# Optimization experiments

Measured on AMD Instinct MI355X. Metric: run time of the kernel, lower is better.

Reference implementation:

```python
import jax, jax.numpy as jnp
import numpy as np

C = 512
C8 = C // 8  # 64
B, H, W = 4, 64, 64


def setup_inputs() -> dict:
    key = jax.random.key(0)
    ks = jax.random.split(key, 8)
    s_in = 1.0 / np.sqrt(C)
    return {
        "x": jax.random.normal(ks[0], (B, C, H, W), dtype=jnp.float32),
        "Wf": jax.random.normal(ks[1], (C8, C), dtype=jnp.float32) * s_in,
        "bf": jax.random.normal(ks[2], (C8,), dtype=jnp.float32) * 0.01,
        "Wg": jax.random.normal(ks[3], (C8, C), dtype=jnp.float32) * s_in,
        "bg": jax.random.normal(ks[4], (C8,), dtype=jnp.float32) * 0.01,
        "Wh": jax.random.normal(ks[5], (C, C), dtype=jnp.float32) * s_in,
        "bh": jax.random.normal(ks[6], (C,), dtype=jnp.float32) * 0.01,
        # original inits gamma=0; use small nonzero so the attention path is exercised
        "gamma": jax.random.normal(ks[7], (1,), dtype=jnp.float32) * 0.1,
    }


def reference(x, Wf, bf, Wg, bg, Wh, bh, gamma):
    b, c, h, w = x.shape
    n = h * w
    xt = x.reshape(b, c, n)  # flatten spatial -> tokens (b, C, N)
    # 1x1 convs are per-token GEMMs
    f = jnp.einsum('bcn,oc->bno', xt, Wf) + bf          # (b, N, C8)
    g = jnp.einsum('bcn,oc->bon', xt, Wg) + bg[:, None]  # (b, C8, N)
    attn = jax.nn.softmax(jnp.einsum('bnk,bkm->bnm', f, g), axis=2)  # (b, N, N)
    hv = jnp.einsum('bcn,oc->bon', xt, Wh) + bh[:, None]  # (b, C, N)
    # torch.bmm(h, attention): out[:,c,j] = sum_i h[:,c,i] * attn[:,i,j]
    sa = jnp.einsum('bci,bij->bcj', hv, attn).reshape(b, c, h, w)
    return gamma[0] * sa + x
```

## Files before the change

### kernel.cpp

```cpp
#include <hip/hip_runtime.h>


#define Bq 4
#define Cq 512
#define Nq 4096

typedef __attribute__((ext_vector_type(8))) short bf16x8;
typedef __attribute__((ext_vector_type(4))) float f32x4;

__device__ __forceinline__ short f2bf(float f) {
  unsigned u = __float_as_uint(f);
  u += 0x7fffu + ((u >> 16) & 1u);
  return (short)(u >> 16);
}
__device__ __forceinline__ float bf2f(short h) {
  return __uint_as_float(((unsigned)(unsigned short)h) << 16);
}

#define MFMA16(A, B, C) __builtin_amdgcn_mfma_f32_16x16x32_bf16((A), (B), (C), 0, 0, 0)

__device__ __forceinline__ size_t fg_frag(int b, int t16, int ss) {
  return ((size_t)((b * 256 + t16) * 2 + ss)) * 512;
}
__device__ __forceinline__ size_t hv_frag(int b, int tc, int si) {
  return ((size_t)((b * 32 + tc) * 128 + si)) * 512;
}
__device__ __forceinline__ size_t p_frag(int b, int jt16, int si) {
  return ((size_t)((b * 256 + jt16) * 128 + si)) * 512;
}

__global__ __launch_bounds__(256) void k_prepw(
    const float* __restrict__ Wf, const float* __restrict__ Wg,
    const float* __restrict__ Wh,
    short* __restrict__ whi, short* __restrict__ wlo, short* __restrict__ whb) {
  int gid = blockIdx.x * 256 + threadIdx.x;
  if (gid < 128 * 512) {
    int row = gid >> 9;
    float v = (row < 64) ? Wf[gid] : Wg[gid - 32768];
    short h = f2bf(v);
    whi[gid] = h;
    wlo[gid] = f2bf(v - bf2f(h));
  }
  whb[gid] = f2bf(Wh[gid]);
}

__global__ __launch_bounds__(256) void k_xpose(
    const float* __restrict__ x, short* __restrict__ xthi, short* __restrict__ xtlo) {
  int b = blockIdx.z, c0 = blockIdx.y * 64, n0 = blockIdx.x * 64;
  __shared__ float tile[64][65];
  int t = threadIdx.x;
  int l = t & 15, g = t >> 4;
  const float* xp = x + ((size_t)b * Cq + c0) * Nq + n0;
#pragma unroll
  for (int e = 0; e < 4; e++) {
    int cl = g + e * 16;
    float4 v = *(const float4*)(xp + (size_t)cl * Nq + l * 4);
    tile[cl][l * 4 + 0] = v.x; tile[cl][l * 4 + 1] = v.y;
    tile[cl][l * 4 + 2] = v.z; tile[cl][l * 4 + 3] = v.w;
  }
  __syncthreads();
#pragma unroll
  for (int e = 0; e < 4; e++) {
    int nl = g + e * 16;
    short hi[4], lo[4];
#pragma unroll
    for (int qq = 0; qq < 4; qq++) {
      float v = tile[l * 4 + qq][nl];
      hi[qq] = f2bf(v);
      lo[qq] = f2bf(v - bf2f(hi[qq]));
    }
    size_t off = ((size_t)b * Nq + n0 + nl) * Cq + c0 + l * 4;
    *(short4*)(xthi + off) = make_short4(hi[0], hi[1], hi[2], hi[3]);
    *(short4*)(xtlo + off) = make_short4(lo[0], lo[1], lo[2], lo[3]);
  }
}

__global__ __launch_bounds__(512) void k_fg(
    const short* __restrict__ xthi, const short* __restrict__ xtlo,
    const short* __restrict__ whi, const short* __restrict__ wlo,
    const float* __restrict__ bfv, const float* __restrict__ bgv,
    short* __restrict__ ffh, short* __restrict__ ffl,
    short* __restrict__ gfh, short* __restrict__ gfl) {
  int b = blockIdx.y, n0 = blockIdx.x * 64;
  int t = threadIdx.x, w = t >> 6, lane = t & 63, l15 = lane & 15, q = lane >> 4;
  int wr = w & 3, wh = w >> 2;
  const short* ah = xthi + ((size_t)b * Nq + n0 + wr * 16 + l15) * Cq;
  const short* al = xtlo + ((size_t)b * Nq + n0 + wr * 16 + l15) * Cq;
  f32x4 z = {0.f, 0.f, 0.f, 0.f};
  f32x4 acc[4] = {z, z, z, z};
  for (int ks = 0; ks < 16; ks++) {
    bf16x8 Ahi = *(const bf16x8*)(ah + ks * 32 + q * 8);
    bf16x8 Alo = *(const bf16x8*)(al + ks * 32 + q * 8);
#pragma unroll
    for (int os = 0; os < 4; os++) {
      int o = wh * 64 + os * 16 + l15;
      bf16x8 Bhi = *(const bf16x8*)(whi + o * 512 + ks * 32 + q * 8);
      bf16x8 Blo = *(const bf16x8*)(wlo + o * 512 + ks * 32 + q * 8);
      acc[os] = MFMA16(Alo, Bhi, acc[os]);
      acc[os] = MFMA16(Ahi, Blo, acc[os]);
      acc[os] = MFMA16(Ahi, Bhi, acc[os]);
    }
  }
#pragma unroll
  for (int os = 0; os < 4; os++) {
#pragma unroll
    for (int r = 0; r < 4; r++) {
      int o = os * 16 + l15;
      int n = n0 + wr * 16 + q * 4 + r;
      float v = acc[os][r] + (wh == 0 ? bfv[o] : bgv[o]);
      size_t off = ((size_t)((b * 256 + (n >> 4)) * 2 + (o >> 5))) * 512
                 + (((o >> 3) & 3) * 16 + (n & 15)) * 8 + (o & 7);
      short h = f2bf(v);
      short lo = f2bf(v - bf2f(h));
      if (wh == 0) { ffh[off] = h; ffl[off] = lo; }
      else         { gfh[off] = h; gfl[off] = lo; }
    }
  }
}

__global__ __launch_bounds__(512) void k_stats(
    const short* __restrict__ ffh, const short* __restrict__ ffl,
    const short* __restrict__ gfh, const short* __restrict__ gfl,
    float* __restrict__ lsum4, short* __restrict__ pmat) {
  int jch = blockIdx.x, jc = jch * 1024, i0 = blockIdx.y * 64, b = blockIdx.z;
  int t = threadIdx.x, w = t >> 6, lane = t & 63, l15 = lane & 15, q = lane >> 4;
  bf16x8 Ahi[4][2], Alo[4][2];
#pragma unroll
  for (int ig = 0; ig < 4; ig++)
#pragma unroll
    for (int ss = 0; ss < 2; ss++) {
      size_t base = fg_frag(b, (i0 >> 4) + ig, ss) + lane * 8;
      Ahi[ig][ss] = *(const bf16x8*)(ffh + base);
      Alo[ig][ss] = *(const bf16x8*)(ffl + base);
    }
  float ls[16];
#pragma unroll
  for (int a = 0; a < 16; a++) ls[a] = 0.f;
  f32x4 z = {0.f, 0.f, 0.f, 0.f};
  for (int jt = 0; jt < 8; jt++) {
    int tj = (jc >> 4) + w * 8 + jt;
    bf16x8 GBh[2], GBl[2];
#pragma unroll
    for (int ss = 0; ss < 2; ss++) {
      size_t base = fg_frag(b, tj, ss) + lane * 8;
      GBh[ss] = *(const bf16x8*)(gfh + base);
      GBl[ss] = *(const bf16x8*)(gfl + base);
    }
#pragma unroll
    for (int ig = 0; ig < 4; ig++) {
      f32x4 sh = z, sl = z;
#pragma unroll
      for (int ss = 0; ss < 2; ss++) {
        sl = MFMA16(Alo[ig][ss], GBh[ss], sl);
        sl = MFMA16(Ahi[ig][ss], GBl[ss], sl);
        sh = MFMA16(Ahi[ig][ss], GBh[ss], sh);
      }
      float ev[4];
#pragma unroll
      for (int r = 0; r < 4; r++) {
        ev[r] = __expf(sh[r] + sl[r]);
        ls[ig * 4 + r] += ev[r];
      }
      uint2 pv;
      pv.x = (unsigned)(unsigned short)f2bf(ev[0]) |
             ((unsigned)(unsigned short)f2bf(ev[1]) << 16);
      pv.y = (unsigned)(unsigned short)f2bf(ev[2]) |
             ((unsigned)(unsigned short)f2bf(ev[3]) << 16);
      size_t pb = p_frag(b, tj, (i0 >> 5) + (ig >> 1)) +
                  (size_t)(((ig & 1) * 2 + (q >> 1)) * 128 + l15 * 8 + (q & 1) * 4);
      *(uint2*)(pmat + pb) = pv;
    }
  }
#pragma unroll
  for (int m = 1; m < 16; m <<= 1) {
#pragma unroll
    for (int a = 0; a < 16; a++) ls[a] += __shfl_xor(ls[a], m, 64);
  }
  __shared__ float part[8][64];
  if (l15 == 0) {
#pragma unroll
    for (int ig = 0; ig < 4; ig++)
#pragma unroll
      for (int r = 0; r < 4; r++) part[w][ig * 16 + q * 4 + r] = ls[ig * 4 + r];
  }
  __syncthreads();
  if (t < 64) {
    float s = 0.f;
#pragma unroll
    for (int ww = 0; ww < 8; ww++) s += part[ww][t];
    lsum4[(size_t)jch * 16384 + (size_t)b * Nq + i0 + t] = s;
  }
}

__global__ __launch_bounds__(512) void k_hv(
    const short* __restrict__ whb, const short* __restrict__ xthi,
    const float* __restrict__ bhv, const float* __restrict__ lsum4,
    short* __restrict__ hvf) {
  int si = blockIdx.x, b = blockIdx.y;
  int t = threadIdx.x, w = t >> 6, lane = t & 63, l15 = lane & 15, q = lane >> 4;
  int c0 = w * 64;
  const short* ar0 = xthi + ((size_t)b * Nq + si * 32 + l15) * Cq;
  const short* ar1 = ar0 + 16 * Cq;
  f32x4 z = {0.f, 0.f, 0.f, 0.f};
  f32x4 acc[2][4];
#pragma unroll
  for (int a = 0; a < 2; a++)
#pragma unroll
    for (int c = 0; c < 4; c++) acc[a][c] = z;
  for (int ks = 0; ks < 16; ks++) {
    bf16x8 A0 = *(const bf16x8*)(ar0 + ks * 32 + q * 8);
    bf16x8 A1 = *(const bf16x8*)(ar1 + ks * 32 + q * 8);
#pragma unroll
    for (int ct = 0; ct < 4; ct++) {
      bf16x8 Bv = *(const bf16x8*)(whb + (size_t)(c0 + ct * 16 + l15) * 512 + ks * 32 + q * 8);
      acc[0][ct] = MFMA16(A0, Bv, acc[0][ct]);
      acc[1][ct] = MFMA16(A1, Bv, acc[1][ct]);
    }
  }
  float li[2][4];
#pragma unroll
  for (int it = 0; it < 2; it++)
#pragma unroll
    for (int r = 0; r < 4; r++) {
      size_t idx = (size_t)b * Nq + si * 32 + it * 16 + q * 4 + r;
      float s = lsum4[idx] + lsum4[16384 + idx] + lsum4[32768 + idx] + lsum4[49152 + idx];
      li[it][r] = 1.0f / s;
    }
  int src0 = ((q & 1) << 5) + l15;
  int src1 = src0 + 16;
  int hiSel = q >> 1;
#pragma unroll
  for (int ct = 0; ct < 4; ct++) {
    float bias = bhv[c0 + ct * 16 + l15];
    unsigned u01[2], u23[2];
#pragma unroll
    for (int it = 0; it < 2; it++) {
      float v0 = (acc[it][ct][0] + bias) * li[it][0];
      float v1 = (acc[it][ct][1] + bias) * li[it][1];
      float v2 = (acc[it][ct][2] + bias) * li[it][2];
      float v3 = (acc[it][ct][3] + bias) * li[it][3];
      u01[it] = (unsigned)(unsigned short)f2bf(v0) | ((unsigned)(unsigned short)f2bf(v1) << 16);
      u23[it] = (unsigned)(unsigned short)f2bf(v2) | ((unsigned)(unsigned short)f2bf(v3) << 16);
    }
    unsigned a0 = __shfl((int)u01[0], src0), b0 = __shfl((int)u01[1], src0);
    unsigned a1 = __shfl((int)u23[0], src0), b1 = __shfl((int)u23[1], src0);
    unsigned a2 = __shfl((int)u01[0], src1), b2 = __shfl((int)u01[1], src1);
    unsigned a3 = __shfl((int)u23[0], src1), b3 = __shfl((int)u23[1], src1);
    uint4 st;
    st.x = hiSel ? b0 : a0;
    st.y = hiSel ? b1 : a1;
    st.z = hiSel ? b2 : a2;
    st.w = hiSel ? b3 : a3;
    *(uint4*)(hvf + hv_frag(b, (c0 >> 4) + ct, si) + (size_t)lane * 8) = st;
  }
}

__global__ __launch_bounds__(512, 4) void k_pv(
    const short* __restrict__ hvf, const short* __restrict__ pmat,
    const float* __restrict__ x, const float* __restrict__ gp,
    float* __restrict__ out) {
  int L = blockIdx.x;
  int combo = L & 7;
  int b = combo >> 1, ch = combo & 1;
  int jt64 = L >> 3;
  int j0 = jt64 * 64;
  int t = threadIdx.x, w = t >> 6, lane = t & 63, l15 = lane & 15, q = lane >> 4;
  int cg = w & 3, jg = w >> 2;
  float gamma = gp[0];
  f32x4 z = {0.f, 0.f, 0.f, 0.f};
  f32x4 acc[4][2];
#pragma unroll
  for (int a = 0; a < 4; a++)
#pragma unroll
    for (int bb = 0; bb < 2; bb++) acc[a][bb] = z;
  const short* hbase = hvf + (size_t)lane * 8;
  const short* pbase = pmat + (size_t)lane * 8;
  int tc0 = ch * 16 + cg * 4;
  int jp0 = (j0 >> 4) + jg * 2;
#pragma unroll 2
  for (int si = 0; si < 128; si++) {
    bf16x8 HV[4], PB[2];
#pragma unroll
    for (int ct = 0; ct < 4; ct++)
      HV[ct] = *(const bf16x8*)(hbase + hv_frag(b, tc0 + ct, si));
#pragma unroll
    for (int jt = 0; jt < 2; jt++)
      PB[jt] = *(const bf16x8*)(pbase + p_frag(b, jp0 + jt, si));
#pragma unroll
    for (int ct = 0; ct < 4; ct++)
#pragma unroll
      for (int jt = 0; jt < 2; jt++)
        acc[ct][jt] = MFMA16(HV[ct], PB[jt], acc[ct][jt]);
  }
#pragma unroll
  for (int ct = 0; ct < 4; ct++) {
#pragma unroll
    for (int jt = 0; jt < 2; jt++) {
#pragma unroll
      for (int r = 0; r < 4; r++) {
        int c = ch * 256 + cg * 64 + ct * 16 + q * 4 + r;
        int j = j0 + jg * 32 + jt * 16 + l15;
        size_t off = ((size_t)b * Cq + c) * Nq + j;
        out[off] = gamma * acc[ct][jt][r] + x[off];
      }
    }
  }
}

extern "C" void kernel_launch(void* const* d_in, const int* in_sizes, int n_in,
                              void* d_out, int out_size, void* d_ws, size_t ws_size,
                              hipStream_t stream) {
  (void)in_sizes; (void)n_in; (void)out_size; (void)ws_size;
  const float* x  = (const float*)d_in[0];
  const float* Wf = (const float*)d_in[1];
  const float* bf = (const float*)d_in[2];
  const float* Wg = (const float*)d_in[3];
  const float* bg = (const float*)d_in[4];
  const float* Wh = (const float*)d_in[5];
  const float* bh = (const float*)d_in[6];
  const float* gm = (const float*)d_in[7];
  float* out = (float*)d_out;
  char* ws = (char*)d_ws;
  short* xthi  = (short*)(ws);
  short* xtlo  = (short*)(ws + 16777216);
  short* ffh   = (short*)(ws + 33554432);
  short* ffl   = (short*)(ws + 35651584);
  short* gfh   = (short*)(ws + 37748736);
  short* gfl   = (short*)(ws + 39845888);
  short* whi   = (short*)(ws + 41943040);
  short* wlo   = (short*)(ws + 42074112);
  short* whb   = (short*)(ws + 42205184);
  float* lsum4 = (float*)(ws + 42729472);
  short* hvf   = (short*)(ws + 42991616);
  short* pmat  = (short*)(ws + 59768832);

  hipLaunchKernelGGL(k_prepw, dim3(1024), dim3(256), 0, stream, Wf, Wg, Wh, whi, wlo, whb);
  hipLaunchKernelGGL(k_xpose, dim3(64, 8, 4), dim3(256), 0, stream, x, xthi, xtlo);
  hipLaunchKernelGGL(k_fg, dim3(64, 4), dim3(512), 0, stream,
                     xthi, xtlo, whi, wlo, bf, bg, ffh, ffl, gfh, gfl);
  hipLaunchKernelGGL(k_stats, dim3(4, 64, 4), dim3(512), 0, stream,
                     ffh, ffl, gfh, gfl, lsum4, pmat);
  hipLaunchKernelGGL(k_hv, dim3(128, 4), dim3(512), 0, stream, whb, xthi, bh, lsum4, hvf);
  hipLaunchKernelGGL(k_pv, dim3(512), dim3(512), 0, stream, hvf, pmat, x, gm, out);
}
```

Measured before the change: 325.8 us.

## Stage k_pv fragments through double-buffered LDS with direct global-to-LDS loads

The P·V kernel now loads the hv and P fragments cooperatively into shared memory with global_load_lds, double-buffered across the reduction steps, and the waves read them back from LDS. Before, each wave fetched its own fragments from global memory, so every fragment was loaded by several waves. Each block's output tile doubles to 128 columns, which halves the grid to 256 blocks and gives 4x4 accumulators per wave, so each loaded fragment is reused more. The cost is two barriers per iteration, fewer blocks (lower occupancy and less parallelism on the device), and more accumulator registers.

```diff
diff --git a/kernel.cpp b/kernel.cpp
--- a/kernel.cpp
+++ b/kernel.cpp
@@ -18,6 +18,12 @@
 }
 
 #define MFMA16(A, B, C) __builtin_amdgcn_mfma_f32_16x16x32_bf16((A), (B), (C), 0, 0, 0)
+
+typedef __attribute__((address_space(1))) const void gas_void;
+typedef __attribute__((address_space(3))) void las_void;
+__device__ __forceinline__ void gl_lds16(const short* g, short* l) {
+  __builtin_amdgcn_global_load_lds((gas_void*)g, (las_void*)l, 16, 0, 0);
+}
 
 __device__ __forceinline__ size_t fg_frag(int b, int t16, int ss) {
   return ((size_t)((b * 256 + t16) * 2 + ss)) * 512;
@@ -255,51 +261,75 @@
   }
 }
 
-__global__ __launch_bounds__(512, 4) void k_pv(
+__global__ __launch_bounds__(512, 2) void k_pv(
     const short* __restrict__ hvf, const short* __restrict__ pmat,
     const float* __restrict__ x, const float* __restrict__ gp,
     float* __restrict__ out) {
   int L = blockIdx.x;
   int combo = L & 7;
   int b = combo >> 1, ch = combo & 1;
-  int jt64 = L >> 3;
-  int j0 = jt64 * 64;
+  int jq = L >> 3;
+  int j0 = jq * 128;
   int t = threadIdx.x, w = t >> 6, lane = t & 63, l15 = lane & 15, q = lane >> 4;
   int cg = w & 3, jg = w >> 2;
+  __shared__ __align__(16) short lds[2][24][512];
   float gamma = gp[0];
   f32x4 z = {0.f, 0.f, 0.f, 0.f};
-  f32x4 acc[4][2];
+  f32x4 acc[4][4];
 #pragma unroll
   for (int a = 0; a < 4; a++)
 #pragma unroll
-    for (int bb = 0; bb < 2; bb++) acc[a][bb] = z;
-  const short* hbase = hvf + (size_t)lane * 8;
-  const short* pbase = pmat + (size_t)lane * 8;
-  int tc0 = ch * 16 + cg * 4;
-  int jp0 = (j0 >> 4) + jg * 2;
-#pragma unroll 2
-  for (int si = 0; si < 128; si++) {
-    bf16x8 HV[4], PB[2];
+    for (int bb = 0; bb < 4; bb++) acc[a][bb] = z;
+
+  int jp0 = j0 >> 4;
+  auto STAGE = [&](int si, int bufIdx) {
+#pragma unroll
+    for (int i = 0; i < 3; i++) {
+      int s = w * 3 + i;
+      const short* src = (s < 16)
+          ? (hvf + hv_frag(b, ch * 16 + s, si))
+          : (pmat + p_frag(b, jp0 + (s - 16), si));
+      gl_lds16(src + (size_t)lane * 8, &lds[bufIdx][s][0]);
+    }
+  };
+  auto COMPUTE = [&](int bufIdx) {
+    bf16x8 HV[4], PB[4];
 #pragma unroll
     for (int ct = 0; ct < 4; ct++)
-      HV[ct] = *(const bf16x8*)(hbase + hv_frag(b, tc0 + ct, si));
-#pragma unroll
-    for (int jt = 0; jt < 2; jt++)
-      PB[jt] = *(const bf16x8*)(pbase + p_frag(b, jp0 + jt, si));
+      HV[ct] = *(const bf16x8*)&lds[bufIdx][cg * 4 + ct][lane * 8];
+#pragma unroll
+    for (int jt = 0; jt < 4; jt++)
+      PB[jt] = *(const bf16x8*)&lds[bufIdx][16 + jg * 4 + jt][lane * 8];
 #pragma unroll
     for (int ct = 0; ct < 4; ct++)
 #pragma unroll
-      for (int jt = 0; jt < 2; jt++)
+      for (int jt = 0; jt < 4; jt++)
         acc[ct][jt] = MFMA16(HV[ct], PB[jt], acc[ct][jt]);
-  }
+  };
+
+  STAGE(0, 0);
+  for (int k = 0; k < 128; k++) {
+    int bi = k & 1;
+    if (k < 127) {
+      STAGE(k + 1, 1 - bi);
+      asm volatile("s_waitcnt vmcnt(3)" ::: "memory");
+    } else {
+      asm volatile("s_waitcnt vmcnt(0)" ::: "memory");
+    }
+    __builtin_amdgcn_s_barrier();
+    COMPUTE(bi);
+    asm volatile("s_waitcnt lgkmcnt(0)" ::: "memory");
+    __builtin_amdgcn_s_barrier();
+  }
+
 #pragma unroll
   for (int ct = 0; ct < 4; ct++) {
 #pragma unroll
-    for (int jt = 0; jt < 2; jt++) {
+    for (int jt = 0; jt < 4; jt++) {
 #pragma unroll
       for (int r = 0; r < 4; r++) {
         int c = ch * 256 + cg * 64 + ct * 16 + q * 4 + r;
-        int j = j0 + jg * 32 + jt * 16 + l15;
+        int j = j0 + jg * 64 + jt * 16 + l15;
         size_t off = ((size_t)b * Cq + c) * Nq + j;
         out[off] = gamma * acc[ct][jt][r] + x[off];
       }
@@ -341,5 +371,5 @@
   hipLaunchKernelGGL(k_stats, dim3(4, 64, 4), dim3(512), 0, stream,
                      ffh, ffl, gfh, gfl, lsum4, pmat);
   hipLaunchKernelGGL(k_hv, dim3(128, 4), dim3(512), 0, stream, whb, xthi, bh, lsum4, hvf);
-  hipLaunchKernelGGL(k_pv, dim3(512), dim3(512), 0, stream, hvf, pmat, x, gm, out);
-}
+  hipLaunchKernelGGL(k_pv, dim3(256), dim3(512), 0, stream, hvf, pmat, x, gm, out);
+}
```

After: 290.2 us. 10.9% less time.
